# Performance work log

Measured on AMD Instinct MI355X. Metric: run time of the kernel, lower is better.

Reference implementation:

```python
import jax, jax.numpy as jnp
import numpy as np

N = 1_000_000
MU_PRIOR = 0.6447


def setup_inputs() -> dict:
    key = jax.random.key(0)
    ks = jax.random.split(key, 8)
    pred_ = jax.random.normal(ks[0], (N, 9), jnp.float32)
    Y_obs = jax.random.normal(ks[1], (N, 9), jnp.float32)
    rrs = jax.random.normal(ks[2], (N, 5), jnp.float32)
    rrs_pred = jax.random.normal(ks[3], (N, 5), jnp.float32)
    nan_array = jax.random.normal(ks[4], (N, 9), jnp.float32)  # all finite -> lens = 9
    # cov_z must be SPD so log(det(cov_z)) is finite
    A = jax.random.normal(ks[5], (N, 3, 3), jnp.float32) * 0.3
    cov_z = jnp.einsum('nij,nkj->nik', A, A) + 0.5 * jnp.eye(3, dtype=jnp.float32)
    mu_z = jax.random.normal(ks[6], (N, 3), jnp.float32)
    parameters = 1.0 + 0.01 * jax.random.normal(ks[7], (64,), jnp.float32)
    return {"pred_": pred_, "Y_obs": Y_obs, "rrs": rrs, "rrs_pred": rrs_pred,
            "nan_array": nan_array, "cov_z": cov_z, "mu_z": mu_z,
            "parameters": parameters}


def reference(pred_, Y_obs, rrs, rrs_pred, nan_array, cov_z, mu_z, parameters):
    n = pred_.shape[0]
    # --- buffers built in __init__ (default multipliers = ones) ---
    se_diag = jnp.asarray([0.0015, 0.0012, 0.001, 0.00086, 0.00057], jnp.float32) ** 2
    rrs_cov_inv = jnp.linalg.inv(jnp.diag(se_diag))            # [5,5]
    Y_cov_inv = jnp.eye(9, dtype=jnp.float32)                  # [9,9]
    s_a = jnp.eye(3, dtype=jnp.float32) * 4.9                  # [3,3]
    s_a_inv = jnp.linalg.inv(s_a)                              # [3,3]

    # trace((X) @ Cinv @ X.T) == sum_n x_n^T Cinv x_n  (trace trick, O(N))
    dr = rrs - rrs_pred                                        # [N,5]
    rrs_error = jnp.einsum('ni,ij,nj->', dr, rrs_cov_inv, dr) / (5.0 * n)

    lens = jnp.sum(~jnp.isnan(nan_array), axis=1).astype(jnp.float32)  # [N]
    dy = pred_ - Y_obs                                         # [N,9]
    obs_quad = jnp.einsum('ni,ij,nj->n', dy, Y_cov_inv, dy)    # [N]
    obs_error = jnp.sum(obs_quad / lens) / n

    # KL(N(mu_z, cov_z) || N(0.6447, s_a)) style term
    logdet_sa = jnp.log(jnp.linalg.det(s_a))
    logdet_cz = jnp.log(jnp.linalg.det(cov_z))                 # [N]
    tr_term = jnp.einsum('ij,nji->n', s_a_inv, cov_z)          # trace(s_a_inv @ cov_z)
    dm = mu_z - MU_PRIOR                                       # [N,3]
    DK = 0.5 * jnp.sum(logdet_sa - logdet_cz + tr_term) / n \
         + 0.5 * jnp.einsum('ni,ij,nj->', dm, s_a_inv, dm) / (3.0 * n)

    l2_norm = jnp.mean((parameters - 1.0) ** 2)
    return rrs_error + 10.0 * obs_error + DK + l2_norm
```

## Files before the change

kernel.cpp:

```cpp
#include <hip/hip_runtime.h>
#include <math.h>

#define MU_PRIOR   0.6447f
#define LOGDET_SA  4.767705615349743f
#define INV_SA     (1.0f/4.9f)

#define CW      64
#define NF4C    144
#define NF4R    80
#define NF4M    48
#define GRID    2048

#define W0 (1.0f / (0.0015f  * 0.0015f))
#define W1 (1.0f / (0.0012f  * 0.0012f))
#define W2 (1.0f / (0.0010f  * 0.0010f))
#define W3 (1.0f / (0.00086f * 0.00086f))
#define W4 (1.0f / (0.00057f * 0.00057f))

__device__ __forceinline__ float warp_reduce_f(float v) {
#pragma unroll
    for (int off = 32; off > 0; off >>= 1) v += __shfl_down(v, off, 64);
    return v;
}

__device__ __forceinline__ double warp_reduce_d(double v) {
#pragma unroll
    for (int off = 32; off > 0; off >>= 1) v += __shfl_down(v, off, 64);
    return v;
}

__device__ __forceinline__ float comb1(float p, float y, float n) {
    const float d = p - y;
    const float d2 = d * d;
    const unsigned u = __float_as_uint(d2) | ((n == n) ? 0u : 0x80000000u);
    return __uint_as_float(u);
}
__device__ __forceinline__ float4 comb4(float4 p, float4 y, float4 n) {
    float4 o;
    o.x = comb1(p.x, y.x, n.x); o.y = comb1(p.y, y.y, n.y);
    o.z = comb1(p.z, y.z, n.z); o.w = comb1(p.w, y.w, n.w);
    return o;
}

__global__ __launch_bounds__(256) void loss_main(
    const float* __restrict__ pred, const float* __restrict__ yobs,
    const float* __restrict__ rrs,  const float* __restrict__ rrsp,
    const float* __restrict__ nanarr, const float* __restrict__ cov,
    const float* __restrict__ mu, double* __restrict__ partial, int nchunks)
{
    __shared__ float4 sV[4 * NF4C];
    __shared__ float4 sC[4 * NF4C];

    const int tid  = threadIdx.x;
    const int lane = tid & 63;
    const int wid  = tid >> 6;
    const int wslot = wid * NF4C;
    const int wgid  = blockIdx.x * 4 + wid;
    const int nw    = (int)gridDim.x * 4;

    const int w0 = (5 - (lane % 5)) % 5;
    float ew[5];
#pragma unroll
    for (int k = 0; k < 5; ++k) {
        int idx = w0 + k; if (idx >= 5) idx -= 5;
        ew[k] = (idx == 0) ? W0 : (idx == 1) ? W1 : (idx == 2) ? W2
               : (idx == 3) ? W3 : W4;
    }

    float acc = 0.0f;

    for (int c = wgid; c < nchunks; c += nw) {
        const float4* gP = reinterpret_cast<const float4*>(pred)   + (size_t)c * NF4C;
        const float4* gY = reinterpret_cast<const float4*>(yobs)   + (size_t)c * NF4C;
        const float4* gN = reinterpret_cast<const float4*>(nanarr) + (size_t)c * NF4C;
        const float4* gC = reinterpret_cast<const float4*>(cov)    + (size_t)c * NF4C;
        const float4* gR = reinterpret_cast<const float4*>(rrs)    + (size_t)c * NF4R;
        const float4* gQ = reinterpret_cast<const float4*>(rrsp)   + (size_t)c * NF4R;
        const float4* gM = reinterpret_cast<const float4*>(mu)     + (size_t)c * NF4M;

        const float4 p0 = gP[lane], p1 = gP[lane + 64];
        const float4 y0 = gY[lane], y1 = gY[lane + 64];
        const float4 n0 = gN[lane], n1 = gN[lane + 64];
        const float4 c0 = gC[lane], c1 = gC[lane + 64];
        const float4 r0 = gR[lane], q0 = gQ[lane];
        float4 p2, y2, n2, c2, r1, q1, m0;
        if (lane < 16) {
            p2 = gP[lane + 128]; y2 = gY[lane + 128];
            n2 = gN[lane + 128]; c2 = gC[lane + 128];
            r1 = gR[lane + 64];  q1 = gQ[lane + 64];
        }
        if (lane < 48) m0 = gM[lane];

        {
            float ra = 0.f;
            const float d0 = r0.x - q0.x, d1 = r0.y - q0.y;
            const float d2 = r0.z - q0.z, d3 = r0.w - q0.w;
            ra += d0 * d0 * ew[0] + d1 * d1 * ew[1]
                + d2 * d2 * ew[2] + d3 * d3 * ew[3];
            if (lane < 16) {
                const float e0 = r1.x - q1.x, e1 = r1.y - q1.y;
                const float e2 = r1.z - q1.z, e3 = r1.w - q1.w;
                ra += e0 * e0 * ew[1] + e1 * e1 * ew[2]
                    + e2 * e2 * ew[3] + e3 * e3 * ew[4];
            }
            acc += ra * 0.2f;
        }

        if (lane < 48) {
            const float d0 = m0.x - MU_PRIOR, d1 = m0.y - MU_PRIOR;
            const float d2 = m0.z - MU_PRIOR, d3 = m0.w - MU_PRIOR;
            acc += (d0 * d0 + d1 * d1 + d2 * d2 + d3 * d3) * (1.0f / 29.4f);
        }

        sV[wslot + lane]       = comb4(p0, y0, n0);
        sV[wslot + lane + 64]  = comb4(p1, y1, n1);
        sC[wslot + lane]       = c0;
        sC[wslot + lane + 64]  = c1;
        if (lane < 16) {
            sV[wslot + lane + 128] = comb4(p2, y2, n2);
            sC[wslot + lane + 128] = c2;
        }

        __builtin_amdgcn_wave_barrier();

        {
            const float* v = reinterpret_cast<const float*>(sV + wslot) + 9 * lane;
            const float* m = reinterpret_cast<const float*>(sC + wslot) + 9 * lane;
            float dy2 = 0.f, len = 0.f;
#pragma unroll
            for (int k = 0; k < 9; ++k) {
                const unsigned u = __float_as_uint(v[k]);
                dy2 += __uint_as_float(u & 0x7fffffffu);
                len += (float)(1u - (u >> 31));
            }
            acc += 10.0f * dy2 / len;

            const float tr  = m[0] + m[4] + m[8];
            const float det = m[0] * (m[4] * m[8] - m[5] * m[7])
                            - m[1] * (m[3] * m[8] - m[5] * m[6])
                            + m[2] * (m[3] * m[7] - m[4] * m[6]);
            acc += 0.5f * (LOGDET_SA - __logf(det) + tr * INV_SA);
        }

        __builtin_amdgcn_wave_barrier();
    }

    acc = warp_reduce_f(acc);
    __shared__ float smem[4];
    if (lane == 0) smem[wid] = acc;
    __syncthreads();
    if (tid == 0)
        partial[blockIdx.x] = (double)(smem[0] + smem[1] + smem[2] + smem[3]);
}

__global__ __launch_bounds__(256) void loss_final(
    const double* __restrict__ partial, int npartials,
    const float* __restrict__ params, int nparams,
    const float* __restrict__ pred, const float* __restrict__ yobs,
    const float* __restrict__ rrs,  const float* __restrict__ rrsp,
    const float* __restrict__ nanarr, const float* __restrict__ cov,
    const float* __restrict__ mu, int mainRows, int rows,
    float* __restrict__ out)
{
    double accA = 0.0;
    double accB = 0.0;

    for (int i = threadIdx.x; i < npartials; i += 256) accA += partial[i];
    for (int i = threadIdx.x; i < nparams; i += 256) {
        const float d = params[i] - 1.0f;
        accB += (double)(d * d);
    }

    for (int r = mainRows + (int)threadIdx.x; r < rows; r += 256) {
        float dy2 = 0.f, len = 0.f;
        for (int i = 0; i < 9; ++i) {
            const float d = pred[9 * (size_t)r + i] - yobs[9 * (size_t)r + i];
            dy2 += d * d;
            const float v = nanarr[9 * (size_t)r + i];
            len += (v == v) ? 1.f : 0.f;
        }
        const float W[5] = {W0, W1, W2, W3, W4};
        float racc = 0.f;
        for (int i = 0; i < 5; ++i) {
            const float d = rrs[5 * (size_t)r + i] - rrsp[5 * (size_t)r + i];
            racc += d * d * W[i];
        }
        const float* m = cov + 9 * (size_t)r;
        const float tr  = m[0] + m[4] + m[8];
        const float det = m[0] * (m[4] * m[8] - m[5] * m[7])
                        - m[1] * (m[3] * m[8] - m[5] * m[6])
                        + m[2] * (m[3] * m[7] - m[4] * m[6]);
        float dm = 0.f;
        for (int i = 0; i < 3; ++i) {
            const float d = mu[3 * (size_t)r + i] - MU_PRIOR;
            dm += d * d;
        }
        accA += (double)(racc * 0.2f + 10.f * dy2 / len
                         + 0.5f * (LOGDET_SA - __logf(det) + tr * INV_SA)
                         + dm * (1.f / 29.4f));
    }

    double val = accA * (1.0 / (double)rows) + accB * (1.0 / (double)nparams);
    val = warp_reduce_d(val);
    __shared__ double sm[4];
    const int lane = threadIdx.x & 63;
    const int wid  = threadIdx.x >> 6;
    if (lane == 0) sm[wid] = val;
    __syncthreads();
    if (threadIdx.x == 0)
        out[0] = (float)(sm[0] + sm[1] + sm[2] + sm[3]);
}

extern "C" void kernel_launch(void* const* d_in, const int* in_sizes, int n_in,
                              void* d_out, int out_size, void* d_ws, size_t ws_size,
                              hipStream_t stream) {
    const float* pred   = (const float*)d_in[0];
    const float* yobs   = (const float*)d_in[1];
    const float* rrs    = (const float*)d_in[2];
    const float* rrsp   = (const float*)d_in[3];
    const float* nanarr = (const float*)d_in[4];
    const float* cov    = (const float*)d_in[5];
    const float* mu     = (const float*)d_in[6];
    const float* params = (const float*)d_in[7];
    float* out = (float*)d_out;

    const int rows     = in_sizes[0] / 9;
    const int nchunks  = rows / CW;
    const int mainRows = nchunks * CW;
    int grid = (nchunks * 4 < GRID * 4) ? ((nchunks + 3) / 4 > 0 ? (nchunks + 3) / 4 : 1) : GRID;
    if (grid > GRID) grid = GRID;

    double* partial = (double*)d_ws;

    loss_main<<<grid, 256, 0, stream>>>(pred, yobs, rrs, rrsp, nanarr,
                                        cov, mu, partial, nchunks);
    loss_final<<<1, 256, 0, stream>>>(partial, grid, params, in_sizes[7],
                                      pred, yobs, rrs, rrsp, nanarr, cov, mu,
                                      mainRows, rows, out);
}
```

Before: 208.1 us.

## Process two rows per thread with direct vector loads instead of LDS transpose

Replaces the wave-cooperative chunk scheme, which did coalesced float4 loads and then transposed through shared memory, with a grid-stride loop where each thread handles a pair of rows. The thread loads 18/10/6 contiguous floats using 4-byte-aligned vector loads. This removes the LDS staging and wave barriers, but each lane now reads a strided 72-byte span, so per-instruction coalescing is worse and the loads may be split because of the alignment. The finalize kernel still handles any odd tail row.

Result: no change. 209.9 us (+0.9%).

```diff
diff --git a/kernel.cpp b/kernel.cpp
--- a/kernel.cpp
+++ b/kernel.cpp
@@ -5,11 +5,7 @@
 #define LOGDET_SA  4.767705615349743f
 #define INV_SA     (1.0f/4.9f)
 
-#define CW      64
-#define NF4C    144
-#define NF4R    80
-#define NF4M    48
-#define GRID    2048
+#define MAXGRID 2048
 
 #define W0 (1.0f / (0.0015f  * 0.0015f))
 #define W1 (1.0f / (0.0012f  * 0.0012f))
@@ -17,6 +13,33 @@
 #define W3 (1.0f / (0.00086f * 0.00086f))
 #define W4 (1.0f / (0.00057f * 0.00057f))
 
+typedef float f4_t __attribute__((ext_vector_type(4)));
+typedef f4_t uf4 __attribute__((aligned(4)));
+typedef float f2_t __attribute__((ext_vector_type(2)));
+typedef f2_t uf2 __attribute__((aligned(4)));
+
+struct R18 { f4_t a, b, c, d; f2_t e; };
+struct R10 { f4_t a, b; f2_t c; };
+struct R6  { f4_t a; f2_t b; };
+
+__device__ __forceinline__ R18 ld18(const float* p) {
+    R18 r;
+    r.a = *(const uf4*)p;        r.b = *(const uf4*)(p + 4);
+    r.c = *(const uf4*)(p + 8);  r.d = *(const uf4*)(p + 12);
+    r.e = *(const uf2*)(p + 16);
+    return r;
+}
+__device__ __forceinline__ R10 ld10(const float* p) {
+    R10 r;
+    r.a = *(const uf4*)p; r.b = *(const uf4*)(p + 4); r.c = *(const uf2*)(p + 8);
+    return r;
+}
+__device__ __forceinline__ R6 ld6(const float* p) {
+    R6 r;
+    r.a = *(const uf4*)p; r.b = *(const uf2*)(p + 4);
+    return r;
+}
+
 __device__ __forceinline__ float warp_reduce_f(float v) {
 #pragma unroll
     for (int off = 32; off > 0; off >>= 1) v += __shfl_down(v, off, 64);
@@ -29,127 +52,99 @@
     return v;
 }
 
-__device__ __forceinline__ float comb1(float p, float y, float n) {
-    const float d = p - y;
-    const float d2 = d * d;
-    const unsigned u = __float_as_uint(d2) | ((n == n) ? 0u : 0x80000000u);
-    return __uint_as_float(u);
-}
-__device__ __forceinline__ float4 comb4(float4 p, float4 y, float4 n) {
-    float4 o;
-    o.x = comb1(p.x, y.x, n.x); o.y = comb1(p.y, y.y, n.y);
-    o.z = comb1(p.z, y.z, n.z); o.w = comb1(p.w, y.w, n.w);
-    return o;
+__device__ __forceinline__ float row_terms(
+    const float p[9], const float y[9], const float a[9], const float c[9],
+    const float r[5], const float q[5], const float m[3])
+{
+    float acc = 0.f;
+    float dy2 = 0.f, len = 0.f;
+#pragma unroll
+    for (int k = 0; k < 9; ++k) {
+        const float d = p[k] - y[k];
+        dy2 += d * d;
+        len += (a[k] == a[k]) ? 1.f : 0.f;
+    }
+    acc += 10.0f * dy2 / len;
+
+    const float tr  = c[0] + c[4] + c[8];
+    const float det = c[0] * (c[4] * c[8] - c[5] * c[7])
+                    - c[1] * (c[3] * c[8] - c[5] * c[6])
+                    + c[2] * (c[3] * c[7] - c[4] * c[6]);
+    acc += 0.5f * (LOGDET_SA - __logf(det) + tr * INV_SA);
+
+    const float W[5] = {W0, W1, W2, W3, W4};
+    float ra = 0.f;
+#pragma unroll
+    for (int k = 0; k < 5; ++k) {
+        const float d = r[k] - q[k];
+        ra += d * d * W[k];
+    }
+    acc += ra * 0.2f;
+
+    float dm = 0.f;
+#pragma unroll
+    for (int k = 0; k < 3; ++k) {
+        const float d = m[k] - MU_PRIOR;
+        dm += d * d;
+    }
+    acc += dm * (1.0f / 29.4f);
+    return acc;
 }
 
 __global__ __launch_bounds__(256) void loss_main(
     const float* __restrict__ pred, const float* __restrict__ yobs,
     const float* __restrict__ rrs,  const float* __restrict__ rrsp,
     const float* __restrict__ nanarr, const float* __restrict__ cov,
-    const float* __restrict__ mu, double* __restrict__ partial, int nchunks)
+    const float* __restrict__ mu, double* __restrict__ partial, int pairs)
 {
-    __shared__ float4 sV[4 * NF4C];
-    __shared__ float4 sC[4 * NF4C];
-
-    const int tid  = threadIdx.x;
-    const int lane = tid & 63;
-    const int wid  = tid >> 6;
-    const int wslot = wid * NF4C;
-    const int wgid  = blockIdx.x * 4 + wid;
-    const int nw    = (int)gridDim.x * 4;
-
-    const int w0 = (5 - (lane % 5)) % 5;
-    float ew[5];
-#pragma unroll
-    for (int k = 0; k < 5; ++k) {
-        int idx = w0 + k; if (idx >= 5) idx -= 5;
-        ew[k] = (idx == 0) ? W0 : (idx == 1) ? W1 : (idx == 2) ? W2
-               : (idx == 3) ? W3 : W4;
-    }
+    const int t0     = blockIdx.x * 256 + threadIdx.x;
+    const int stride = (int)gridDim.x * 256;
 
     float acc = 0.0f;
 
-    for (int c = wgid; c < nchunks; c += nw) {
-        const float4* gP = reinterpret_cast<const float4*>(pred)   + (size_t)c * NF4C;
-        const float4* gY = reinterpret_cast<const float4*>(yobs)   + (size_t)c * NF4C;
-        const float4* gN = reinterpret_cast<const float4*>(nanarr) + (size_t)c * NF4C;
-        const float4* gC = reinterpret_cast<const float4*>(cov)    + (size_t)c * NF4C;
-        const float4* gR = reinterpret_cast<const float4*>(rrs)    + (size_t)c * NF4R;
-        const float4* gQ = reinterpret_cast<const float4*>(rrsp)   + (size_t)c * NF4R;
-        const float4* gM = reinterpret_cast<const float4*>(mu)     + (size_t)c * NF4M;
-
-        const float4 p0 = gP[lane], p1 = gP[lane + 64];
-        const float4 y0 = gY[lane], y1 = gY[lane + 64];
-        const float4 n0 = gN[lane], n1 = gN[lane + 64];
-        const float4 c0 = gC[lane], c1 = gC[lane + 64];
-        const float4 r0 = gR[lane], q0 = gQ[lane];
-        float4 p2, y2, n2, c2, r1, q1, m0;
-        if (lane < 16) {
-            p2 = gP[lane + 128]; y2 = gY[lane + 128];
-            n2 = gN[lane + 128]; c2 = gC[lane + 128];
-            r1 = gR[lane + 64];  q1 = gQ[lane + 64];
-        }
-        if (lane < 48) m0 = gM[lane];
+#pragma unroll 1
+    for (int t = t0; t < pairs; t += stride) {
+        const size_t b9 = 18ull * (size_t)t;
+        const size_t b5 = 10ull * (size_t)t;
+        const size_t b3 =  6ull * (size_t)t;
+
+        const R18 P = ld18(pred   + b9);
+        const R18 Y = ld18(yobs   + b9);
+        const R18 A = ld18(nanarr + b9);
+        const R18 C = ld18(cov    + b9);
+        const R10 R = ld10(rrs    + b5);
+        const R10 Q = ld10(rrsp   + b5);
+        const R6  M = ld6 (mu     + b3);
 
         {
-            float ra = 0.f;
-            const float d0 = r0.x - q0.x, d1 = r0.y - q0.y;
-            const float d2 = r0.z - q0.z, d3 = r0.w - q0.w;
-            ra += d0 * d0 * ew[0] + d1 * d1 * ew[1]
-                + d2 * d2 * ew[2] + d3 * d3 * ew[3];
-            if (lane < 16) {
-                const float e0 = r1.x - q1.x, e1 = r1.y - q1.y;
-                const float e2 = r1.z - q1.z, e3 = r1.w - q1.w;
-                ra += e0 * e0 * ew[1] + e1 * e1 * ew[2]
-                    + e2 * e2 * ew[3] + e3 * e3 * ew[4];
-            }
-            acc += ra * 0.2f;
-        }
-
-        if (lane < 48) {
-            const float d0 = m0.x - MU_PRIOR, d1 = m0.y - MU_PRIOR;
-            const float d2 = m0.z - MU_PRIOR, d3 = m0.w - MU_PRIOR;
-            acc += (d0 * d0 + d1 * d1 + d2 * d2 + d3 * d3) * (1.0f / 29.4f);
-        }
-
-        sV[wslot + lane]       = comb4(p0, y0, n0);
-        sV[wslot + lane + 64]  = comb4(p1, y1, n1);
-        sC[wslot + lane]       = c0;
-        sC[wslot + lane + 64]  = c1;
-        if (lane < 16) {
-            sV[wslot + lane + 128] = comb4(p2, y2, n2);
-            sC[wslot + lane + 128] = c2;
-        }
-
-        __builtin_amdgcn_wave_barrier();
-
+            const float p[9] = {P.a.x,P.a.y,P.a.z,P.a.w,P.b.x,P.b.y,P.b.z,P.b.w,P.c.x};
+            const float y[9] = {Y.a.x,Y.a.y,Y.a.z,Y.a.w,Y.b.x,Y.b.y,Y.b.z,Y.b.w,Y.c.x};
+            const float a[9] = {A.a.x,A.a.y,A.a.z,A.a.w,A.b.x,A.b.y,A.b.z,A.b.w,A.c.x};
+            const float c[9] = {C.a.x,C.a.y,C.a.z,C.a.w,C.b.x,C.b.y,C.b.z,C.b.w,C.c.x};
+            const float r[5] = {R.a.x,R.a.y,R.a.z,R.a.w,R.b.x};
+            const float q[5] = {Q.a.x,Q.a.y,Q.a.z,Q.a.w,Q.b.x};
+            const float m[3] = {M.a.x,M.a.y,M.a.z};
+            acc += row_terms(p, y, a, c, r, q, m);
+        }
         {
-            const float* v = reinterpret_cast<const float*>(sV + wslot) + 9 * lane;
-            const float* m = reinterpret_cast<const float*>(sC + wslot) + 9 * lane;
-            float dy2 = 0.f, len = 0.f;
-#pragma unroll
-            for (int k = 0; k < 9; ++k) {
-                const unsigned u = __float_as_uint(v[k]);
-                dy2 += __uint_as_float(u & 0x7fffffffu);
-                len += (float)(1u - (u >> 31));
-            }
-            acc += 10.0f * dy2 / len;
-
-            const float tr  = m[0] + m[4] + m[8];
-            const float det = m[0] * (m[4] * m[8] - m[5] * m[7])
-                            - m[1] * (m[3] * m[8] - m[5] * m[6])
-                            + m[2] * (m[3] * m[7] - m[4] * m[6]);
-            acc += 0.5f * (LOGDET_SA - __logf(det) + tr * INV_SA);
-        }
-
-        __builtin_amdgcn_wave_barrier();
+            const float p[9] = {P.c.y,P.c.z,P.c.w,P.d.x,P.d.y,P.d.z,P.d.w,P.e.x,P.e.y};
+            const float y[9] = {Y.c.y,Y.c.z,Y.c.w,Y.d.x,Y.d.y,Y.d.z,Y.d.w,Y.e.x,Y.e.y};
+            const float a[9] = {A.c.y,A.c.z,A.c.w,A.d.x,A.d.y,A.d.z,A.d.w,A.e.x,A.e.y};
+            const float c[9] = {C.c.y,C.c.z,C.c.w,C.d.x,C.d.y,C.d.z,C.d.w,C.e.x,C.e.y};
+            const float r[5] = {R.b.y,R.b.z,R.b.w,R.c.x,R.c.y};
+            const float q[5] = {Q.b.y,Q.b.z,Q.b.w,Q.c.x,Q.c.y};
+            const float m[3] = {M.a.w,M.b.x,M.b.y};
+            acc += row_terms(p, y, a, c, r, q, m);
+        }
     }
 
     acc = warp_reduce_f(acc);
     __shared__ float smem[4];
+    const int lane = threadIdx.x & 63;
+    const int wid  = threadIdx.x >> 6;
     if (lane == 0) smem[wid] = acc;
     __syncthreads();
-    if (tid == 0)
+    if (threadIdx.x == 0)
         partial[blockIdx.x] = (double)(smem[0] + smem[1] + smem[2] + smem[3]);
 }
 
@@ -225,15 +220,17 @@
     float* out = (float*)d_out;
 
     const int rows     = in_sizes[0] / 9;
-    const int nchunks  = rows / CW;
-    const int mainRows = nchunks * CW;
-    int grid = (nchunks * 4 < GRID * 4) ? ((nchunks + 3) / 4 > 0 ? (nchunks + 3) / 4 : 1) : GRID;
-    if (grid > GRID) grid = GRID;
+    const int pairs    = rows / 2;
+    const int mainRows = pairs * 2;
+
+    int grid = (pairs + 255) / 256;
+    if (grid > MAXGRID) grid = MAXGRID;
+    if (grid < 1) grid = 1;
 
     double* partial = (double*)d_ws;
 
     loss_main<<<grid, 256, 0, stream>>>(pred, yobs, rrs, rrsp, nanarr,
-                                        cov, mu, partial, nchunks);
+                                        cov, mu, partial, pairs);
     loss_final<<<1, 256, 0, stream>>>(partial, grid, params, in_sizes[7],
                                       pred, yobs, rrs, rrsp, nanarr, cov, mu,
                                       mainRows, rows, out);
```
